# Optimization experiments

Measured on AMD Instinct MI355X. Metric: run time of the kernel, lower is better.

## Reference

```python
import jax, jax.numpy as jnp
import numpy as np

N_DIMS = 4          # len(dims): gauge-link channels split off by unpack_x
N_BANDS = 3         # SU(3) matrices
THRESHOLD = 1e-3    # trnorm_threshold
LAYER_CH = [6, 12, 12]  # input_channels + args.layer_channels


def cplx_einsum(eq, a, b):
    # complex einsum on real/imag-stacked tensors (last dim = 2)
    ar, ai = a[..., 0], a[..., 1]
    br, bi = b[..., 0], b[..., 1]
    re = jnp.einsum(eq, ar, br) - jnp.einsum(eq, ai, bi)
    im = jnp.einsum(eq, ar, bi) + jnp.einsum(eq, ai, br)
    return jnp.stack((re, im), axis=-1)


def h_conj(w):
    # hermitian conjugate: transpose matrix dims, negate imag part
    wt = jnp.swapaxes(w, -3, -2)
    return jnp.stack((wt[..., 0], -wt[..., 1]), axis=-1)


def gebl(x, weight):
    # x: [b, X, n_dims + n_in, nb, nb, 2]; weight: [n_out, w_in, w_in, 2]
    u, w = x[:, :, :N_DIMS], x[:, :, N_DIMS:]
    w = jnp.concatenate((w, h_conj(w)), axis=2)            # conjugation enlargement
    b, s = w.shape[0], w.shape[1]
    eye = jnp.zeros((N_BANDS, N_BANDS, 2), w.dtype).at[..., 0].set(jnp.eye(N_BANDS, dtype=w.dtype))
    unit = jnp.broadcast_to(eye, (b, s, 1, N_BANDS, N_BANDS, 2))
    w = jnp.concatenate((w, unit), axis=2)                 # unit elements
    ww = cplx_einsum('bxvij,bxwjk->bxvwik', w, w)          # pairwise matrix products
    w_out = cplx_einsum('uvw,bxvwij->bxuij', weight, ww)   # channel mixing
    return jnp.concatenate((u, w_out), axis=2)


def gerelu(x):
    u, w = x[:, :, :N_DIMS], x[:, :, N_DIMS:]
    tr_re = jnp.einsum('bxwiic->bxwc', w)[..., 0]          # Re(Tr W)
    w = jax.nn.relu(tr_re)[..., None, None, None] * w
    return jnp.concatenate((u, w), axis=2)


def trnorm(x):
    # trnorm_on_abs = True branch
    u, w = x[:, :, :N_DIMS], x[:, :, N_DIMS:]
    tr = jnp.einsum('bxviic->bxvc', w)
    tr_abs = jnp.sqrt(tr[..., 0] ** 2 + tr[..., 1] ** 2)
    norm = jnp.maximum(jnp.mean(tr_abs, axis=2), THRESHOLD)
    w = w / norm[:, :, None, None, None, None]
    return jnp.concatenate((u, w), axis=2)


def setup_inputs() -> dict:
    key = jax.random.key(0)
    ks = jax.random.split(key, 5)
    b, X = 2, 8 * 8 * 8 * 8
    x = jax.random.normal(ks[0], (b, X, N_DIMS + LAYER_CH[0], N_BANDS, N_BANDS, 2), jnp.float32)
    # GEBL weights: [n_out, w_in, w_in, 2], w_in = 2*n_in + 1
    w_in1 = 2 * LAYER_CH[0] + 1  # 13
    w_in2 = 2 * LAYER_CH[1] + 1  # 25
    w1 = jax.random.normal(ks[1], (LAYER_CH[1], w_in1, w_in1, 2), jnp.float32) * 0.1
    w2 = jax.random.normal(ks[2], (LAYER_CH[2], w_in2, w_in2, 2), jnp.float32) * 0.1
    dense_w = jax.random.normal(ks[3], (1, LAYER_CH[2] * 2), jnp.float32) * 0.2
    dense_b = jax.random.normal(ks[4], (1,), jnp.float32) * 0.01
    return {"x": x, "w1": w1, "w2": w2, "dense_w": dense_w, "dense_b": dense_b}


def reference(x, w1, w2, dense_w, dense_b):
    # GEBL -> GEReLU -> TrNorm (trnorm_before_ReLU=False), twice
    h = trnorm(gerelu(gebl(x, w1)))
    h = trnorm(gerelu(gebl(h, w2)))
    # Trace (normalized) -> reshape -> dense -> reshape
    w = h[:, :, N_DIMS:]
    tr = (1.0 / N_BANDS) * jnp.einsum('bxwiic->bxwc', w)   # [b, X, c, 2]
    flat = tr.reshape(-1, tr.shape[2] * 2)                 # torch .view: (c,2) interleaved
    out = flat @ dense_w.T + dense_b                        # [b*X, 1]
    return out.reshape(x.shape[0], -1)                      # [b, num_sites]
```

## Files before the change

kernel.cpp:

```cpp
#include <hip/hip_runtime.h>
#include <math.h>


#define NPTS 8192
#define THRESH 0.001f

__global__ void geblnet_setup(const float* __restrict__ w2,
                              float4* __restrict__ CTt) {
    int j = blockIdx.x * blockDim.x + threadIdx.x;
    if (j >= 12 * 169) return;
    int u = j / 169, it = j % 169;
    const float* W = w2 + u * 25 * 25 * 2;
#define WR(v, w) W[((v) * 25 + (w)) * 2]
#define WI(v, w) W[((v) * 25 + (w)) * 2 + 1]
    float c0, c1, c2, c3;
    if (it < 78) {
        int q = it, a = 0;
        while (q >= 12 - a) { q -= 12 - a; ++a; }
        int b = a + q;
        float ar = WR(a, b) + (a != b ? WR(b, a) : 0.f);
        float ai = WI(a, b) + (a != b ? WI(b, a) : 0.f);
        float br = WR(12 + a, 12 + b) + (a != b ? WR(12 + b, 12 + a) : 0.f);
        float bi = WI(12 + a, 12 + b) + (a != b ? WI(12 + b, 12 + a) : 0.f);
        c0 = ar + br; c1 = bi - ai; c2 = ai + bi; c3 = ar - br;
    } else if (it < 156) {
        int q = it - 78, a = 0;
        while (q >= 12 - a) { q -= 12 - a; ++a; }
        int b = a + q;
        if (a != b) {
            float gr = WR(a, 12 + b) + WR(12 + b, a);
            float gi = WI(a, 12 + b) + WI(12 + b, a);
            float dr = WR(b, 12 + a) + WR(12 + a, b);
            float di = WI(b, 12 + a) + WI(12 + a, b);
            c0 = gr + dr; c1 = di - gi; c2 = gi + di; c3 = gr - dr;
        } else {
            float er = WR(a, 12 + a) + WR(12 + a, a);
            float ei = WI(a, 12 + a) + WI(12 + a, a);
            c0 = er; c1 = 0.f; c2 = ei; c3 = 0.f;
        }
    } else if (it < 168) {
        int a = it - 156;
        float fr = WR(a, 24) + WR(24, a), fi = WI(a, 24) + WI(24, a);
        float pr = WR(12 + a, 24) + WR(24, 12 + a);
        float pi = WI(12 + a, 24) + WI(24, 12 + a);
        c0 = fr + pr; c1 = pi - fi; c2 = fi + pi; c3 = fr - pr;
    } else {
        c0 = 3.f * WR(24, 24); c1 = 0.f; c2 = 3.f * WI(24, 24); c3 = 0.f;
    }
    CTt[it * 12 + u] = make_float4(c0, c1, c2, c3);
#undef WR
#undef WI
}

union Scr {
    float2 bs[702];
    struct {
        float2 tpar[60];
        float2 tr1[12];
        float  sc1[12];
        float  gb[12];
        float  tra[12];
    } s;
};

__global__ __launch_bounds__(64) void geblnet_main(
    const float2* __restrict__ x2,
    const float2* __restrict__ w1g,
    const float* __restrict__ dw,
    const float* __restrict__ db,
    const float4* __restrict__ CTt,
    float* __restrict__ out)
{
    __shared__ float2 WeGV[170];
    __shared__ Scr S;
    __shared__ float2 Hs[108];

    const int t = threadIdx.x;
    const int p = blockIdx.x;

    for (int j = t; j < 117; j += 64) {
        int v = j / 9, ik = j - v * 9;
        int i = ik / 3, jj = ik - i * 3;
        float2 val;
        if (v < 6) val = x2[(size_t)p * 90 + (4 + v) * 9 + ik];
        else if (v < 12) {
            float2 s = x2[(size_t)p * 90 + (v - 2) * 9 + jj * 3 + i];
            val = make_float2(s.x, -s.y);
        } else val = make_float2((i == jj) ? 1.f : 0.f, 0.f);
        WeGV[v * 10 + ik] = val;
    }
    __syncthreads();

    #pragma unroll 1
    for (int g = 0; g < 2; ++g) {
        const int u0 = g * 6;
        #pragma unroll 1
        for (int e = t; e < 702; e += 64) {
            int uu = e / 117, rem = e - uu * 117;
            int v = rem / 9, jk = rem - v * 9;
            const float2* cp = w1g + ((u0 + uu) * 13 + v) * 13;
            float br = 0.f, bi = 0.f;
            #pragma unroll
            for (int w = 0; w < 13; ++w) {
                float2 cc = cp[w];
                float2 ee = WeGV[w * 10 + jk];
                br += cc.x * ee.x - cc.y * ee.y;
                bi += cc.x * ee.y + cc.y * ee.x;
            }
            S.bs[(uu * 13 + v) * 9 + jk] = make_float2(br, bi);
        }
        __syncthreads();
        if (t < 54) {
            int uu = t / 9, ik = t - uu * 9;
            int i = ik / 3, k = ik - i * 3;
            float hr = 0.f, hi = 0.f;
            #pragma unroll
            for (int v = 0; v < 13; ++v) {
                const float2* a = &WeGV[v * 10 + i * 3];
                const float2* b = &S.bs[(uu * 13 + v) * 9 + k];
                #pragma unroll
                for (int j = 0; j < 3; ++j) {
                    float2 aj = a[j];
                    float2 bj = b[j * 3];
                    hr += aj.x * bj.x - aj.y * bj.y;
                    hi += aj.x * bj.y + aj.y * bj.x;
                }
            }
            Hs[(u0 + uu) * 9 + ik] = make_float2(hr, hi);
        }
        __syncthreads();
    }

    if (t < 12) {
        float2 a = Hs[t * 9 + 0], b = Hs[t * 9 + 4], c = Hs[t * 9 + 8];
        float2 tt = make_float2(a.x + b.x + c.x, a.y + b.y + c.y);
        S.s.tr1[t] = tt;
        float gg = tt.x > 0.f ? tt.x : 0.f;
        S.s.gb[t] = gg;
        S.s.tra[t] = gg * sqrtf(tt.x * tt.x + tt.y * tt.y);
    }
    __syncthreads();
    if (t < 12) {
        float m = 0.f;
        #pragma unroll
        for (int u = 0; u < 12; ++u) m += S.s.tra[u];
        S.s.sc1[t] = S.s.gb[t] / fmaxf(m * (1.f / 12.f), THRESH);
    }
    __syncthreads();

    for (int it = t; it < 169; it += 64) {
        float2 val;
        if (it < 156) {
            int q = it < 78 ? it : it - 78;
            float fs = sqrtf(625.0f - 8.0f * (float)q);
            int a = (int)((25.0f - fs) * 0.5f);
            int b = q - (a * (25 - a)) / 2 + a;
            const float2* Ha = &Hs[a * 9];
            const float2* Hb = &Hs[b * 9];
            float s = S.s.sc1[a] * S.s.sc1[b];
            float vr = 0.f, vi = 0.f;
            if (it < 78) {
                #pragma unroll
                for (int i = 0; i < 3; ++i)
                    #pragma unroll
                    for (int jj = 0; jj < 3; ++jj) {
                        float2 A = Ha[i * 3 + jj], B = Hb[jj * 3 + i];
                        vr += A.x * B.x - A.y * B.y;
                        vi += A.x * B.y + A.y * B.x;
                    }
            } else {
                #pragma unroll
                for (int e = 0; e < 9; ++e) {
                    float2 A = Ha[e], B = Hb[e];
                    vr += A.x * B.x + A.y * B.y;
                    vi += A.y * B.x - A.x * B.y;
                }
            }
            val = make_float2(s * vr, s * vi);
        } else if (it < 168) {
            int a = it - 156;
            float s = S.s.sc1[a]; float2 tt = S.s.tr1[a];
            val = make_float2(s * tt.x, s * tt.y);
        } else {
            val = make_float2(1.f, 0.f);
        }
        WeGV[it] = val;
    }
    __syncthreads();

    if (t < 60) {
        int q = t / 12, u = t - q * 12;
        int i0 = q * 34, i1 = (q == 4) ? 169 : i0 + 34;
        float tre = 0.f, tim = 0.f;
        for (int it = i0; it < i1; ++it) {
            float4 c = CTt[it * 12 + u];
            float2 gv = WeGV[it];
            tre += c.x * gv.x + c.y * gv.y;
            tim += c.z * gv.x + c.w * gv.y;
        }
        S.s.tpar[u * 5 + q] = make_float2(tre, tim);
    }
    __syncthreads();

    if (t < 12) {
        float2 tt = make_float2(0.f, 0.f);
        #pragma unroll
        for (int q = 0; q < 5; ++q) {
            float2 A = S.s.tpar[t * 5 + q];
            tt.x += A.x; tt.y += A.y;
        }
        S.s.tr1[t] = tt;
        float g = tt.x > 0.f ? tt.x : 0.f;
        S.s.gb[t] = g;
        S.s.tra[t] = g * sqrtf(tt.x * tt.x + tt.y * tt.y);
    }
    __syncthreads();
    if (t == 0) {
        float m = 0.f;
        #pragma unroll
        for (int u = 0; u < 12; ++u) m += S.s.tra[u];
        float inv = 1.f / fmaxf(m * (1.f / 12.f), THRESH);
        float acc = db[0];
        #pragma unroll
        for (int u = 0; u < 12; ++u) {
            float s = S.s.gb[u] * inv * (1.f / 3.f);
            acc += s * (S.s.tr1[u].x * dw[2 * u] + S.s.tr1[u].y * dw[2 * u + 1]);
        }
        out[p] = acc;
    }
}

extern "C" void kernel_launch(void* const* d_in, const int* in_sizes, int n_in,
                              void* d_out, int out_size, void* d_ws, size_t ws_size,
                              hipStream_t stream) {
    const float* x  = (const float*)d_in[0];
    const float* w1 = (const float*)d_in[1];
    const float* w2 = (const float*)d_in[2];
    const float* dw = (const float*)d_in[3];
    const float* db = (const float*)d_in[4];
    float* outp = (float*)d_out;
    float4* CTt = (float4*)d_ws;

    geblnet_setup<<<(12 * 169 + 255) / 256, 256, 0, stream>>>(w2, CTt);

    geblnet_main<<<NPTS, 64, 0, stream>>>(
        (const float2*)x, (const float2*)w1, dw, db, CTt, outp);
}
```

Baseline: 133.5 us.

## Register-block first GEBL, warp-shuffle reductions, prefetch CTt coefficients

Each thread in the first GEBL channel-mixing stage now computes three adjacent output elements, so one weight load is reused across three shared-memory reads. The trace-norm mean and the final dense reduction now use 16-lane shuffle reductions instead of shared-memory arrays and extra barriers, which removes several __syncthreads. The first four CTt coefficients are loaded into registers before the WeGV build so global latency overlaps other work. This adds register pressure and leaves most lanes idle during the shuffles.

```diff
diff --git a/kernel.cpp b/kernel.cpp
--- a/kernel.cpp
+++ b/kernel.cpp
@@ -58,8 +58,6 @@
         float2 tpar[60];
         float2 tr1[12];
         float  sc1[12];
-        float  gb[12];
-        float  tra[12];
     } s;
 };
 
@@ -95,19 +93,30 @@
     for (int g = 0; g < 2; ++g) {
         const int u0 = g * 6;
         #pragma unroll 1
-        for (int e = t; e < 702; e += 64) {
-            int uu = e / 117, rem = e - uu * 117;
-            int v = rem / 9, jk = rem - v * 9;
+        for (int j = t; j < 234; j += 64) {
+            int row = j / 3;
+            int d0 = (j - row * 3) * 3;
+            int uu = row / 13;
+            int v = row - uu * 13;
             const float2* cp = w1g + ((u0 + uu) * 13 + v) * 13;
-            float br = 0.f, bi = 0.f;
+            float ar0 = 0.f, ai0 = 0.f, ar1 = 0.f, ai1 = 0.f;
+            float ar2 = 0.f, ai2 = 0.f;
             #pragma unroll
             for (int w = 0; w < 13; ++w) {
                 float2 cc = cp[w];
-                float2 ee = WeGV[w * 10 + jk];
-                br += cc.x * ee.x - cc.y * ee.y;
-                bi += cc.x * ee.y + cc.y * ee.x;
-            }
-            S.bs[(uu * 13 + v) * 9 + jk] = make_float2(br, bi);
+                const float2* wr = &WeGV[w * 10 + d0];
+                float2 e0 = wr[0], e1 = wr[1], e2 = wr[2];
+                ar0 += cc.x * e0.x - cc.y * e0.y;
+                ai0 += cc.x * e0.y + cc.y * e0.x;
+                ar1 += cc.x * e1.x - cc.y * e1.y;
+                ai1 += cc.x * e1.y + cc.y * e1.x;
+                ar2 += cc.x * e2.x - cc.y * e2.y;
+                ai2 += cc.x * e2.y + cc.y * e2.x;
+            }
+            float2* bp = &S.bs[(uu * 13 + v) * 9 + d0];
+            bp[0] = make_float2(ar0, ai0);
+            bp[1] = make_float2(ar1, ai1);
+            bp[2] = make_float2(ar2, ai2);
         }
         __syncthreads();
         if (t < 54) {
@@ -131,22 +140,35 @@
         __syncthreads();
     }
 
-    if (t < 12) {
-        float2 a = Hs[t * 9 + 0], b = Hs[t * 9 + 4], c = Hs[t * 9 + 8];
-        float2 tt = make_float2(a.x + b.x + c.x, a.y + b.y + c.y);
-        S.s.tr1[t] = tt;
-        float gg = tt.x > 0.f ? tt.x : 0.f;
-        S.s.gb[t] = gg;
-        S.s.tra[t] = gg * sqrtf(tt.x * tt.x + tt.y * tt.y);
-    }
-    __syncthreads();
-    if (t < 12) {
-        float m = 0.f;
-        #pragma unroll
-        for (int u = 0; u < 12; ++u) m += S.s.tra[u];
-        S.s.sc1[t] = S.s.gb[t] / fmaxf(m * (1.f / 12.f), THRESH);
-    }
-    __syncthreads();
+    {
+        float2 tt = make_float2(0.f, 0.f);
+        float gg = 0.f, tra_v = 0.f;
+        if (t < 12) {
+            float2 a = Hs[t * 9 + 0], b = Hs[t * 9 + 4], c = Hs[t * 9 + 8];
+            tt = make_float2(a.x + b.x + c.x, a.y + b.y + c.y);
+            gg = tt.x > 0.f ? tt.x : 0.f;
+            tra_v = gg * sqrtf(tt.x * tt.x + tt.y * tt.y);
+        }
+        float m = tra_v;
+        m += __shfl_xor(m, 1, 16);
+        m += __shfl_xor(m, 2, 16);
+        m += __shfl_xor(m, 4, 16);
+        m += __shfl_xor(m, 8, 16);
+        if (t < 12) {
+            S.s.tr1[t] = tt;
+            S.s.sc1[t] = gg / fmaxf(m * (1.f / 12.f), THRESH);
+        }
+    }
+    __syncthreads();
+
+    const int q5 = t / 12, u5 = t - q5 * 12;
+    const int i0 = q5 * 34;
+    const bool act5 = (t < 60);
+    const int pbase = act5 ? i0 * 12 + u5 : 0;
+    float4 pc0 = CTt[pbase];
+    float4 pc1 = CTt[pbase + 12];
+    float4 pc2 = CTt[pbase + 24];
+    float4 pc3 = CTt[pbase + 36];
 
     for (int it = t; it < 169; it += 64) {
         float2 val;
@@ -188,45 +210,57 @@
     }
     __syncthreads();
 
-    if (t < 60) {
-        int q = t / 12, u = t - q * 12;
-        int i0 = q * 34, i1 = (q == 4) ? 169 : i0 + 34;
-        float tre = 0.f, tim = 0.f;
-        for (int it = i0; it < i1; ++it) {
-            float4 c = CTt[it * 12 + u];
+    if (act5) {
+        const int i1 = (q5 == 4) ? 169 : i0 + 34;
+        float2 g0 = WeGV[i0], g1 = WeGV[i0 + 1];
+        float2 g2 = WeGV[i0 + 2], g3 = WeGV[i0 + 3];
+        float tre = pc0.x * g0.x + pc0.y * g0.y
+                  + pc1.x * g1.x + pc1.y * g1.y
+                  + pc2.x * g2.x + pc2.y * g2.y
+                  + pc3.x * g3.x + pc3.y * g3.y;
+        float tim = pc0.z * g0.x + pc0.w * g0.y
+                  + pc1.z * g1.x + pc1.w * g1.y
+                  + pc2.z * g2.x + pc2.w * g2.y
+                  + pc3.z * g3.x + pc3.w * g3.y;
+        #pragma unroll 4
+        for (int it = i0 + 4; it < i1; ++it) {
+            float4 c = CTt[it * 12 + u5];
             float2 gv = WeGV[it];
             tre += c.x * gv.x + c.y * gv.y;
             tim += c.z * gv.x + c.w * gv.y;
         }
-        S.s.tpar[u * 5 + q] = make_float2(tre, tim);
-    }
-    __syncthreads();
-
-    if (t < 12) {
+        S.s.tpar[u5 * 5 + q5] = make_float2(tre, tim);
+    }
+    __syncthreads();
+
+    {
         float2 tt = make_float2(0.f, 0.f);
-        #pragma unroll
-        for (int q = 0; q < 5; ++q) {
-            float2 A = S.s.tpar[t * 5 + q];
-            tt.x += A.x; tt.y += A.y;
-        }
-        S.s.tr1[t] = tt;
-        float g = tt.x > 0.f ? tt.x : 0.f;
-        S.s.gb[t] = g;
-        S.s.tra[t] = g * sqrtf(tt.x * tt.x + tt.y * tt.y);
-    }
-    __syncthreads();
-    if (t == 0) {
-        float m = 0.f;
-        #pragma unroll
-        for (int u = 0; u < 12; ++u) m += S.s.tra[u];
-        float inv = 1.f / fmaxf(m * (1.f / 12.f), THRESH);
-        float acc = db[0];
-        #pragma unroll
-        for (int u = 0; u < 12; ++u) {
-            float s = S.s.gb[u] * inv * (1.f / 3.f);
-            acc += s * (S.s.tr1[u].x * dw[2 * u] + S.s.tr1[u].y * dw[2 * u + 1]);
-        }
-        out[p] = acc;
+        float gg = 0.f, tra_v = 0.f;
+        if (t < 12) {
+            #pragma unroll
+            for (int q = 0; q < 5; ++q) {
+                float2 A = S.s.tpar[t * 5 + q];
+                tt.x += A.x; tt.y += A.y;
+            }
+            gg = tt.x > 0.f ? tt.x : 0.f;
+            tra_v = gg * sqrtf(tt.x * tt.x + tt.y * tt.y);
+        }
+        float m = tra_v;
+        m += __shfl_xor(m, 1, 16);
+        m += __shfl_xor(m, 2, 16);
+        m += __shfl_xor(m, 4, 16);
+        m += __shfl_xor(m, 8, 16);
+        float term = 0.f;
+        if (t < 12) {
+            float inv = 1.f / fmaxf(m * (1.f / 12.f), THRESH);
+            float s = gg * inv * (1.f / 3.f);
+            term = s * (tt.x * dw[2 * t] + tt.y * dw[2 * t + 1]);
+        }
+        term += __shfl_xor(term, 1, 16);
+        term += __shfl_xor(term, 2, 16);
+        term += __shfl_xor(term, 4, 16);
+        term += __shfl_xor(term, 8, 16);
+        if (t == 0) out[p] = term + db[0];
     }
 }
 
```

Result: faster. 125.4 us (-6.1%).
